# Performance work log

Measured on AMD Instinct MI355X. Metric: run time of the kernel, lower is better.

The kernel has to match this reference:

```python
import jax, jax.numpy as jnp
import numpy as np

NUM_HEADS = 16
BIG_NEG = -1e9  # additive mask value for padded keys (fp32)


def setup_inputs() -> dict:
    key = jax.random.key(0)
    ks = jax.random.split(key, 12)
    T, S, B, E = 2048, 2048, 2, 1024
    bound = np.sqrt(6.0 / (E + E))  # xavier_uniform for square E x E weights
    inp = {
        'query': jax.random.normal(ks[0], (T, B, E), jnp.float32),
        'key': jax.random.normal(ks[1], (S, B, E), jnp.float32),
        'value': jax.random.normal(ks[2], (S, B, E), jnp.float32),
        'attn_mask': jax.random.normal(ks[3], (T, S), jnp.float32) * 0.1,
        'key_padding_mask': jnp.zeros((B, S), dtype=bool),
        'Wq': jax.random.uniform(ks[4], (E, E), jnp.float32, -bound, bound),
        'bq': jnp.zeros((E,), jnp.float32),
        'Wk': jax.random.uniform(ks[5], (E, E), jnp.float32, -bound, bound),
        'bk': jnp.zeros((E,), jnp.float32),
        'Wv': jax.random.uniform(ks[6], (E, E), jnp.float32, -bound, bound),
        'bv': jnp.zeros((E,), jnp.float32),
        'Wo': jax.random.uniform(ks[7], (E, E), jnp.float32, -bound, bound),
        'bo': jnp.zeros((E,), jnp.float32),
    }
    return inp


def reference(query, key, value, attn_mask, key_padding_mask,
              Wq, bq, Wk, bk, Wv, bv, Wo, bo):
    T, B, E = query.shape
    S = key.shape[0]
    H = NUM_HEADS
    d = E // H
    scale = 1.0 / jnp.sqrt(jnp.asarray(d, query.dtype))

    # projections (nn.Linear: x @ W.T + b), then split heads
    q = (query @ Wq.T + bq).reshape(T, B, H, d) * scale  # [T,B,H,d]
    k = (key @ Wk.T + bk).reshape(S, B, H, d)            # [S,B,H,d]
    v = (value @ Wv.T + bv).reshape(S, B, H, d)          # [S,B,H,d]

    # QK^T scores: [B,H,T,S]
    scores = jnp.einsum('tbhd,sbhd->bhts', q, k)

    # merge masks: additive attn_mask + key_padding_mask (True -> -inf)
    merged = attn_mask[None, None, :, :] + jnp.where(
        key_padding_mask[:, None, None, :], BIG_NEG, 0.0).astype(scores.dtype)
    scores = scores + merged

    attn = jax.nn.softmax(scores, axis=-1)  # dropout p=0 -> identity

    out = jnp.einsum('bhts,sbhd->tbhd', attn, v).reshape(T, B, E)
    return out @ Wo.T + bo  # [T,B,E]
```

## Files before the change

kernel.cpp:

```cpp
#include <hip/hip_runtime.h>
#include <hip/hip_bf16.h>

typedef unsigned short u16;
typedef __attribute__((ext_vector_type(8))) short bf16x8;
typedef __attribute__((ext_vector_type(4))) float f32x4;

#define T_DIM 2048
#define S_DIM 2048
#define B_DIM 2
#define E_DIM 1024
#define H_DIM 16
#define D_HEAD 64
#define NTOK 4096

#if __has_builtin(__builtin_amdgcn_exp2f)
#define EXP2F(x) __builtin_amdgcn_exp2f(x)
#else
#define EXP2F(x) exp2f(x)
#endif

#define GLL16(gp, lp) __builtin_amdgcn_global_load_lds((gp), (lp), 16, 0, 0)

__device__ __forceinline__ float bf2f(u16 u) {
  union { unsigned int i; float f; } v; v.i = ((unsigned int)u) << 16; return v.f;
}
__device__ __forceinline__ u16 f2bf(float f) {
  union { float f; unsigned int i; } v; v.f = f;
  unsigned int r = v.i + 0x7fffu + ((v.i >> 16) & 1u);
  return (u16)(r >> 16);
}
__device__ __forceinline__ unsigned pk2(float a, float b) {
  return (unsigned)f2bf(a) | ((unsigned)f2bf(b) << 16);
}
__device__ __forceinline__ float bfu_lo(unsigned w) {
  union { unsigned int i; float f; } v; v.i = w << 16; return v.f;
}
__device__ __forceinline__ float bfu_hi(unsigned w) {
  union { unsigned int i; float f; } v; v.i = w & 0xffff0000u; return v.f;
}
__device__ __forceinline__ uint4 loadA8(const void* A, size_t base, int bf) {
  if (bf) return *(const uint4*)&((const u16*)A)[base];
  const float* af = (const float*)A + base;
  uint4 r;
  r.x = pk2(af[0], af[1]); r.y = pk2(af[2], af[3]);
  r.z = pk2(af[4], af[5]); r.w = pk2(af[6], af[7]);
  return r;
}

__global__ void detect_dtype(const u16* q, int* flag) {
  int lane = threadIdx.x;
  float v = bf2f(q[2 * lane]);
  bool ok = (v < 16.f) && (v > -16.f);
  unsigned long long b = __ballot(ok);
  if (lane == 0) *flag = (b == ~0ull) ? 1 : 0;
}

__global__ void prep_params(const void* Wq, const void* Wk, const void* Wv, const void* Wo,
                            const void* bq, const void* bk, const void* bv, const void* bo,
                            u16* wqkv, u16* wo, float* b3, float* bof,
                            const int* flag) {
  const int bf = *flag;
  const int W = E_DIM * E_DIM;
  int idx = blockIdx.x * 256 + threadIdx.x;
  if (idx < 4 * W) {
    int which = idx / W, i = idx - which * W;
    const void* src = which == 0 ? Wq : which == 1 ? Wk : which == 2 ? Wv : Wo;
    float v = bf ? bf2f(((const u16*)src)[i]) : ((const float*)src)[i];
    if (which == 0) v *= 0.125f;
    if (which < 3) wqkv[idx] = f2bf(v);
    else           wo[i] = f2bf(v);
  } else {
    int j = idx - 4 * W;
    if (j < 4 * E_DIM) {
      int which = j / E_DIM, i = j - which * E_DIM;
      const void* src = which == 0 ? bq : which == 1 ? bk : which == 2 ? bv : bo;
      float v = bf ? bf2f(((const u16*)src)[i]) : ((const float*)src)[i];
      if (which == 0) v *= 0.125f;
      if (which < 3) b3[j] = v;
      else           bof[i] = v;
    }
  }
}

__launch_bounds__(256)
__global__ void conv_in(const void* __restrict__ Q, const void* __restrict__ K,
                        const void* __restrict__ V,
                        u16* __restrict__ qb, u16* __restrict__ kb,
                        u16* __restrict__ vb, const int* __restrict__ flag) {
  const int bf = *flag;
  const size_t W = (size_t)NTOK * E_DIM;
  size_t e8 = ((size_t)blockIdx.x * 256 + threadIdx.x) * 8;
  int which = (int)(e8 / W);
  size_t i = e8 - (size_t)which * W;
  const void* src = which == 0 ? Q : which == 1 ? K : V;
  u16* dst = which == 0 ? qb : which == 1 ? kb : vb;
  *(uint4*)&dst[i] = loadA8(src, i, bf);
}

__global__ void prep_mask(const void* mask, const unsigned char* kpm,
                          u16* Mc, const int* flag) {
  const float L2E = 1.44269504f;
  const int bf = *flag;
  size_t e8 = ((size_t)blockIdx.x * 256 + threadIdx.x) * 8;
  int b = (int)(e8 / ((size_t)T_DIM * S_DIM));
  size_t rem = e8 - (size_t)b * T_DIM * S_DIM;
  int t = (int)(rem / S_DIM), s = (int)(rem - (size_t)t * S_DIM);
  const unsigned char* kb = &kpm[(size_t)b * S_DIM + s];
  uint4 o;
  if (bf) {
    const u16* m8 = &((const u16*)mask)[(size_t)t * S_DIM + s];
    o.x = pk2((bf2f(m8[0]) + (kb[0] ? -1e9f : 0.f)) * L2E,
              (bf2f(m8[1]) + (kb[1] ? -1e9f : 0.f)) * L2E);
    o.y = pk2((bf2f(m8[2]) + (kb[2] ? -1e9f : 0.f)) * L2E,
              (bf2f(m8[3]) + (kb[3] ? -1e9f : 0.f)) * L2E);
    o.z = pk2((bf2f(m8[4]) + (kb[4] ? -1e9f : 0.f)) * L2E,
              (bf2f(m8[5]) + (kb[5] ? -1e9f : 0.f)) * L2E);
    o.w = pk2((bf2f(m8[6]) + (kb[6] ? -1e9f : 0.f)) * L2E,
              (bf2f(m8[7]) + (kb[7] ? -1e9f : 0.f)) * L2E);
  } else {
    const float* mf = (const float*)mask + (size_t)t * S_DIM + s;
    o.x = pk2((mf[0] + (kb[0] ? -1e9f : 0.f)) * L2E,
              (mf[1] + (kb[1] ? -1e9f : 0.f)) * L2E);
    o.y = pk2((mf[2] + (kb[2] ? -1e9f : 0.f)) * L2E,
              (mf[3] + (kb[3] ? -1e9f : 0.f)) * L2E);
    o.z = pk2((mf[4] + (kb[4] ? -1e9f : 0.f)) * L2E,
              (mf[5] + (kb[5] ? -1e9f : 0.f)) * L2E);
    o.w = pk2((mf[6] + (kb[6] ? -1e9f : 0.f)) * L2E,
              (mf[7] + (kb[7] ? -1e9f : 0.f)) * L2E);
  }
  *(uint4*)&Mc[e8] = o;
}

__launch_bounds__(256)
__global__ void transpose_v(const u16* __restrict__ vp, u16* __restrict__ vt) {
  __shared__ unsigned int t[64 * 65];
  const int tid = threadIdx.x;
  const int s0 = blockIdx.x * 64;
  const int bh = blockIdx.y;
  const int b = bh / H_DIM, h = bh % H_DIM;
  {
    int sr = tid >> 2, cq = (tid & 3) * 16;
    const u16* src = &vp[((size_t)(s0 + sr) * B_DIM + b) * E_DIM + h * 64 + cq];
#pragma unroll
    for (int j = 0; j < 16; j++) t[(cq + j) * 65 + sr] = src[j];
  }
  __syncthreads();
  {
    int d = tid >> 2, sq = (tid & 3) * 16;
    u16* dst = &vt[((size_t)bh * 64 + d) * S_DIM + s0 + sq];
    uint4 o0, o1;
    o0.x = (t[d*65+sq+0] & 0xffffu) | (t[d*65+sq+1] << 16);
    o0.y = (t[d*65+sq+2] & 0xffffu) | (t[d*65+sq+3] << 16);
    o0.z = (t[d*65+sq+4] & 0xffffu) | (t[d*65+sq+5] << 16);
    o0.w = (t[d*65+sq+6] & 0xffffu) | (t[d*65+sq+7] << 16);
    o1.x = (t[d*65+sq+8] & 0xffffu) | (t[d*65+sq+9] << 16);
    o1.y = (t[d*65+sq+10] & 0xffffu) | (t[d*65+sq+11] << 16);
    o1.z = (t[d*65+sq+12] & 0xffffu) | (t[d*65+sq+13] << 16);
    o1.w = (t[d*65+sq+14] & 0xffffu) | (t[d*65+sq+15] << 16);
    *(uint4*)&dst[0] = o0;
    *(uint4*)&dst[8] = o1;
  }
}

__launch_bounds__(256, 3)
__global__ void gemm_qkv(const u16* __restrict__ Qb2, const u16* __restrict__ Kb2,
                         const u16* __restrict__ Vb2, const u16* __restrict__ W3,
                         const float* __restrict__ b3,
                         u16* __restrict__ qp, u16* __restrict__ kp, u16* __restrict__ vp) {
  __shared__ alignas(16) u16 As[128 * 64];
  __shared__ alignas(16) u16 Bs[128 * 64];
  const int tid = threadIdx.x;
  const int wave = tid >> 6, lane = tid & 63;
  const int g = lane >> 4, c = lane & 15;
  const int wy = wave >> 1, wx = wave & 1;
  const int which = blockIdx.x >> 3;
  const u16* A = which == 0 ? Qb2 : which == 1 ? Kb2 : Vb2;
  u16* dst = which == 0 ? qp : which == 1 ? kp : vp;
  const int m0 = blockIdx.y * 128, n0 = blockIdx.x * 128;
  const int K = E_DIM;

  const int swr = lane >> 3;
  const int swb = (lane & 7) ^ swr;
  const u16* Ag = &A [(size_t)(m0 + wave * 8 + swr) * K + swb * 8];
  const u16* Bg = &W3[(size_t)(n0 + wave * 8 + swr) * K + swb * 8];

  f32x4 acc[4][4] = {};
  for (int kc = 0; kc < K; kc += 64) {
#pragma unroll
    for (int i = 0; i < 4; i++) {
      GLL16(&Ag[(size_t)(i * 32) * K + kc], &As[(wave * 8 + i * 32) * 64]);
      GLL16(&Bg[(size_t)(i * 32) * K + kc], &Bs[(wave * 8 + i * 32) * 64]);
    }
    __syncthreads();
#pragma unroll
    for (int ks = 0; ks < 2; ks++) {
      const int kb = (((ks << 2) | g) ^ (c & 7)) * 8;
      bf16x8 av0 = *(const bf16x8*)&As[(wy * 64 +  0 + c) * 64 + kb];
      bf16x8 av1 = *(const bf16x8*)&As[(wy * 64 + 16 + c) * 64 + kb];
      bf16x8 av2 = *(const bf16x8*)&As[(wy * 64 + 32 + c) * 64 + kb];
      bf16x8 av3 = *(const bf16x8*)&As[(wy * 64 + 48 + c) * 64 + kb];
      bf16x8 bv0 = *(const bf16x8*)&Bs[(wx * 64 +  0 + c) * 64 + kb];
      bf16x8 bv1 = *(const bf16x8*)&Bs[(wx * 64 + 16 + c) * 64 + kb];
      bf16x8 bv2 = *(const bf16x8*)&Bs[(wx * 64 + 32 + c) * 64 + kb];
      bf16x8 bv3 = *(const bf16x8*)&Bs[(wx * 64 + 48 + c) * 64 + kb];
      acc[0][0] = __builtin_amdgcn_mfma_f32_16x16x32_bf16(av0, bv0, acc[0][0], 0, 0, 0);
      acc[0][1] = __builtin_amdgcn_mfma_f32_16x16x32_bf16(av0, bv1, acc[0][1], 0, 0, 0);
      acc[0][2] = __builtin_amdgcn_mfma_f32_16x16x32_bf16(av0, bv2, acc[0][2], 0, 0, 0);
      acc[0][3] = __builtin_amdgcn_mfma_f32_16x16x32_bf16(av0, bv3, acc[0][3], 0, 0, 0);
      acc[1][0] = __builtin_amdgcn_mfma_f32_16x16x32_bf16(av1, bv0, acc[1][0], 0, 0, 0);
      acc[1][1] = __builtin_amdgcn_mfma_f32_16x16x32_bf16(av1, bv1, acc[1][1], 0, 0, 0);
      acc[1][2] = __builtin_amdgcn_mfma_f32_16x16x32_bf16(av1, bv2, acc[1][2], 0, 0, 0);
      acc[1][3] = __builtin_amdgcn_mfma_f32_16x16x32_bf16(av1, bv3, acc[1][3], 0, 0, 0);
      acc[2][0] = __builtin_amdgcn_mfma_f32_16x16x32_bf16(av2, bv0, acc[2][0], 0, 0, 0);
      acc[2][1] = __builtin_amdgcn_mfma_f32_16x16x32_bf16(av2, bv1, acc[2][1], 0, 0, 0);
      acc[2][2] = __builtin_amdgcn_mfma_f32_16x16x32_bf16(av2, bv2, acc[2][2], 0, 0, 0);
      acc[2][3] = __builtin_amdgcn_mfma_f32_16x16x32_bf16(av2, bv3, acc[2][3], 0, 0, 0);
      acc[3][0] = __builtin_amdgcn_mfma_f32_16x16x32_bf16(av3, bv0, acc[3][0], 0, 0, 0);
      acc[3][1] = __builtin_amdgcn_mfma_f32_16x16x32_bf16(av3, bv1, acc[3][1], 0, 0, 0);
      acc[3][2] = __builtin_amdgcn_mfma_f32_16x16x32_bf16(av3, bv2, acc[3][2], 0, 0, 0);
      acc[3][3] = __builtin_amdgcn_mfma_f32_16x16x32_bf16(av3, bv3, acc[3][3], 0, 0, 0);
    }
    __syncthreads();
  }
#pragma unroll
  for (int mi = 0; mi < 4; mi++)
#pragma unroll
    for (int ni = 0; ni < 4; ni++)
#pragma unroll
      for (int r = 0; r < 4; r++) {
        int row = m0 + wy * 64 + mi * 16 + g * 4 + r;
        int col = n0 + wx * 64 + ni * 16 + c;
        int inner = col & (E_DIM - 1);
        dst[(size_t)row * E_DIM + inner] = f2bf(acc[mi][ni][r] + b3[col]);
      }
}

__launch_bounds__(256, 2)
__global__ void gemm_o(const u16* __restrict__ Aa, const u16* __restrict__ Bw,
                       const float* __restrict__ bias, void* __restrict__ C,
                       int out_f32) {
  __shared__ alignas(16) u16 As[64 * 64];
  __shared__ alignas(16) u16 Bs[128 * 64];
  const int tid = threadIdx.x;
  const int wave = tid >> 6, lane = tid & 63;
  const int g = lane >> 4, c = lane & 15;
  const int wy = wave >> 1, wx = wave & 1;
  const int m0 = blockIdx.y * 64, n0 = blockIdx.x * 128;
  const int K = E_DIM, N = E_DIM;

  const int swr = lane >> 3;
  const int swb = (lane & 7) ^ swr;
  const u16* Ag = &Aa[(size_t)(m0 + wave * 8 + swr) * K + swb * 8];
  const u16* Bg = &Bw[(size_t)(n0 + wave * 8 + swr) * K + swb * 8];

  f32x4 acc[2][4] = {};
  for (int kc = 0; kc < K; kc += 64) {
#pragma unroll
    for (int i = 0; i < 2; i++)
      GLL16(&Ag[(size_t)(i * 32) * K + kc], &As[(wave * 8 + i * 32) * 64]);
#pragma unroll
    for (int i = 0; i < 4; i++)
      GLL16(&Bg[(size_t)(i * 32) * K + kc], &Bs[(wave * 8 + i * 32) * 64]);
    __syncthreads();
#pragma unroll
    for (int ks = 0; ks < 2; ks++) {
      const int kb = (((ks << 2) | g) ^ (c & 7)) * 8;
      bf16x8 av0 = *(const bf16x8*)&As[(wy * 32 +  0 + c) * 64 + kb];
      bf16x8 av1 = *(const bf16x8*)&As[(wy * 32 + 16 + c) * 64 + kb];
      bf16x8 bv0 = *(const bf16x8*)&Bs[(wx * 64 +  0 + c) * 64 + kb];
      bf16x8 bv1 = *(const bf16x8*)&Bs[(wx * 64 + 16 + c) * 64 + kb];
      bf16x8 bv2 = *(const bf16x8*)&Bs[(wx * 64 + 32 + c) * 64 + kb];
      bf16x8 bv3 = *(const bf16x8*)&Bs[(wx * 64 + 48 + c) * 64 + kb];
      acc[0][0] = __builtin_amdgcn_mfma_f32_16x16x32_bf16(av0, bv0, acc[0][0], 0, 0, 0);
      acc[0][1] = __builtin_amdgcn_mfma_f32_16x16x32_bf16(av0, bv1, acc[0][1], 0, 0, 0);
      acc[0][2] = __builtin_amdgcn_mfma_f32_16x16x32_bf16(av0, bv2, acc[0][2], 0, 0, 0);
      acc[0][3] = __builtin_amdgcn_mfma_f32_16x16x32_bf16(av0, bv3, acc[0][3], 0, 0, 0);
      acc[1][0] = __builtin_amdgcn_mfma_f32_16x16x32_bf16(av1, bv0, acc[1][0], 0, 0, 0);
      acc[1][1] = __builtin_amdgcn_mfma_f32_16x16x32_bf16(av1, bv1, acc[1][1], 0, 0, 0);
      acc[1][2] = __builtin_amdgcn_mfma_f32_16x16x32_bf16(av1, bv2, acc[1][2], 0, 0, 0);
      acc[1][3] = __builtin_amdgcn_mfma_f32_16x16x32_bf16(av1, bv3, acc[1][3], 0, 0, 0);
    }
    __syncthreads();
  }
#pragma unroll
  for (int mi = 0; mi < 2; mi++)
#pragma unroll
    for (int ni = 0; ni < 4; ni++)
#pragma unroll
      for (int r = 0; r < 4; r++) {
        int row = m0 + wy * 32 + mi * 16 + g * 4 + r;
        int col = n0 + wx * 64 + ni * 16 + c;
        float v = acc[mi][ni][r] + bias[col];
        size_t idx = (size_t)row * N + col;
        if (out_f32) ((float*)C)[idx] = v;
        else         ((u16*)C)[idx] = f2bf(v);
      }
}

__launch_bounds__(256, 4)
__global__ void flash_attn(const u16* __restrict__ Qb, const u16* __restrict__ Kb,
                           const u16* __restrict__ Vtg, const u16* __restrict__ Mc,
                           u16* __restrict__ ctx) {
  __shared__ alignas(16) u16 Ks[64 * 72];
  __shared__ alignas(16) u16 Vs[64 * 72];
  __shared__ alignas(16) u16 MP[64 * 72];
  const int tid = threadIdx.x;
  const int wave = tid >> 6, lane = tid & 63;
  const int g = lane >> 4, c = lane & 15;
  const int bh = blockIdx.x;
  const int t0 = blockIdx.y * 64;
  const int b = bh / H_DIM, h = bh % H_DIM;
  const size_t hoff = (size_t)h * D_HEAD;
  const float L2E = 1.44269504f;
  const u16* mc = &Mc[((size_t)b * T_DIM + t0) * S_DIM];
  const int rr = tid >> 3, oo = (tid & 7) * 8;

  *(uint4*)&Ks[(rr)      * 72 + oo] =
      *(const uint4*)&Qb[((size_t)(t0 + rr)      * B_DIM + b) * E_DIM + hoff + oo];
  *(uint4*)&Ks[(rr + 32) * 72 + oo] =
      *(const uint4*)&Qb[((size_t)(t0 + rr + 32) * B_DIM + b) * E_DIM + hoff + oo];
  __syncthreads();
  const int arow = wave * 16 + c;
  bf16x8 q0 = *(const bf16x8*)&Ks[arow * 72 + g * 8];
  bf16x8 q1 = *(const bf16x8*)&Ks[arow * 72 + 32 + g * 8];

  uint4 pk0, pk1, pv0, pv1, pm0, pm1;
  pk0 = *(const uint4*)&Kb[((size_t)(rr)      * B_DIM + b) * E_DIM + hoff + oo];
  pk1 = *(const uint4*)&Kb[((size_t)(rr + 32) * B_DIM + b) * E_DIM + hoff + oo];
  pv0 = *(const uint4*)&Vtg[((size_t)bh * 64 + rr)      * S_DIM + oo];
  pv1 = *(const uint4*)&Vtg[((size_t)bh * 64 + rr + 32) * S_DIM + oo];
  pm0 = *(const uint4*)&mc[(size_t)(rr)      * S_DIM + oo];
  pm1 = *(const uint4*)&mc[(size_t)(rr + 32) * S_DIM + oo];
  __syncthreads();

  f32x4 O[4] = {};
  float rsum = 0.f;
  const int trow = arow * 72;

  for (int s0 = 0; s0 < S_DIM; s0 += 64) {
    *(uint4*)&Ks[(rr)      * 72 + oo] = pk0;
    *(uint4*)&Ks[(rr + 32) * 72 + oo] = pk1;
    *(uint4*)&Vs[(rr)      * 72 + oo] = pv0;
    *(uint4*)&Vs[(rr + 32) * 72 + oo] = pv1;
    *(uint4*)&MP[(rr)      * 72 + oo] = pm0;
    *(uint4*)&MP[(rr + 32) * 72 + oo] = pm1;
    __syncthreads();
    if (s0 + 64 < S_DIM) {
      int s2 = s0 + 64;
      pk0 = *(const uint4*)&Kb[((size_t)(s2 + rr)      * B_DIM + b) * E_DIM + hoff + oo];
      pk1 = *(const uint4*)&Kb[((size_t)(s2 + rr + 32) * B_DIM + b) * E_DIM + hoff + oo];
      pv0 = *(const uint4*)&Vtg[((size_t)bh * 64 + rr)      * S_DIM + s2 + oo];
      pv1 = *(const uint4*)&Vtg[((size_t)bh * 64 + rr + 32) * S_DIM + s2 + oo];
      pm0 = *(const uint4*)&mc[(size_t)(rr)      * S_DIM + s2 + oo];
      pm1 = *(const uint4*)&mc[(size_t)(rr + 32) * S_DIM + s2 + oo];
    }

    f32x4 sc[4] = {};
#pragma unroll
    for (int n = 0; n < 4; n++) {
      bf16x8 k0 = *(const bf16x8*)&Ks[(n * 16 + c) * 72 + g * 8];
      bf16x8 k1 = *(const bf16x8*)&Ks[(n * 16 + c) * 72 + 32 + g * 8];
      sc[n] = __builtin_amdgcn_mfma_f32_16x16x32_bf16(k0, q0, sc[n], 0, 0, 0);
      sc[n] = __builtin_amdgcn_mfma_f32_16x16x32_bf16(k1, q1, sc[n], 0, 0, 0);
    }
#pragma unroll
    for (int n = 0; n < 4; n++) {
      uint2 mw = *(const uint2*)&MP[trow + n * 16 + g * 4];
      float p0 = EXP2F(fmaf(sc[n][0], L2E, bfu_lo(mw.x)));
      float p1 = EXP2F(fmaf(sc[n][1], L2E, bfu_hi(mw.x)));
      float p2 = EXP2F(fmaf(sc[n][2], L2E, bfu_lo(mw.y)));
      float p3 = EXP2F(fmaf(sc[n][3], L2E, bfu_hi(mw.y)));
      rsum += (p0 + p1) + (p2 + p3);
      *(unsigned*)&MP[trow + n * 16 + g * 4]     = pk2(p0, p1);
      *(unsigned*)&MP[trow + n * 16 + g * 4 + 2] = pk2(p2, p3);
    }
    bf16x8 p0 = *(const bf16x8*)&MP[arow * 72 + g * 8];
    bf16x8 p1 = *(const bf16x8*)&MP[arow * 72 + 32 + g * 8];
#pragma unroll
    for (int n = 0; n < 4; n++) {
      bf16x8 v0 = *(const bf16x8*)&Vs[(n * 16 + c) * 72 + g * 8];
      bf16x8 v1 = *(const bf16x8*)&Vs[(n * 16 + c) * 72 + 32 + g * 8];
      O[n] = __builtin_amdgcn_mfma_f32_16x16x32_bf16(p0, v0, O[n], 0, 0, 0);
      O[n] = __builtin_amdgcn_mfma_f32_16x16x32_bf16(p1, v1, O[n], 0, 0, 0);
    }
    __syncthreads();
  }
  float l = rsum;
  l += __shfl_xor(l, 16, 64);
  l += __shfl_xor(l, 32, 64);
  float rl = 1.f / l;
#pragma unroll
  for (int r = 0; r < 4; r++) {
    float rlr = __shfl(rl, g * 4 + r, 64);
    int t = t0 + wave * 16 + g * 4 + r;
#pragma unroll
    for (int n = 0; n < 4; n++) {
      int dcol = n * 16 + c;
      ctx[((size_t)t * B_DIM + b) * E_DIM + hoff + dcol] = f2bf(O[n][r] * rlr);
    }
  }
}

extern "C" void kernel_launch(void* const* d_in, const int* in_sizes, int n_in,
                              void* d_out, int out_size, void* d_ws, size_t ws_size,
                              hipStream_t stream) {
  const void* query = d_in[0];
  const void* key   = d_in[1];
  const void* value = d_in[2];
  const void* amask = d_in[3];
  const unsigned char* kpm = (const unsigned char*)d_in[4];
  const void* Wq = d_in[5];  const void* bq = d_in[6];
  const void* Wk = d_in[7];  const void* bk = d_in[8];
  const void* Wv = d_in[9];  const void* bv = d_in[10];
  const void* Wo = d_in[11]; const void* bo = d_in[12];

  int out_f32 = 0;
  {
    hipDeviceptr_t base = nullptr; size_t sz = 0;
    if (hipMemGetAddressRange(&base, &sz, (hipDeviceptr_t)d_out) == hipSuccess && sz) {
      size_t avail = sz - (size_t)((char*)d_out - (char*)base);
      size_t need_f32 = (size_t)out_size * 4;
      if (avail >= need_f32 && avail <= need_f32 + need_f32 / 2) out_f32 = 1;
    }
  }

  char* ws = (char*)d_ws;
  size_t off = 0;
  auto alloc = [&](size_t bytes) {
    void* p = ws + off;
    off += (bytes + 255) & ~(size_t)255;
    return p;
  };
  int*   flag = (int*)  alloc(256);
  u16*   qp   = (u16*)  alloc((size_t)NTOK * E_DIM * 2);
  u16*   kp   = (u16*)  alloc((size_t)NTOK * E_DIM * 2);
  u16*   vp   = (u16*)  alloc((size_t)NTOK * E_DIM * 2);
  u16*   vt   = (u16*)  alloc((size_t)NTOK * E_DIM * 2);
  u16*   Mcb  = (u16*)  alloc((size_t)B_DIM * T_DIM * S_DIM * 2);
  u16*   wqkv = (u16*)  alloc((size_t)3 * E_DIM * E_DIM * 2);
  u16*   wo   = (u16*)  alloc((size_t)E_DIM * E_DIM * 2);
  float* b3   = (float*)alloc(3 * E_DIM * 4);
  float* bof  = (float*)alloc(E_DIM * 4);
  if (off > ws_size) return;

  u16* qb  = vt;
  u16* kb2 = Mcb;
  u16* vb2 = Mcb + (size_t)NTOK * E_DIM;

  detect_dtype<<<1, 64, 0, stream>>>((const u16*)query, flag);

  {
    int total = 4 * E_DIM * E_DIM + 4 * E_DIM;
    prep_params<<<(total + 255) / 256, 256, 0, stream>>>(
        Wq, Wk, Wv, Wo, bq, bk, bv, bo, wqkv, wo, b3, bof, flag);
  }

  {
    size_t total8 = (size_t)3 * NTOK * E_DIM / 8;
    conv_in<<<(unsigned)(total8 / 256), 256, 0, stream>>>(
        query, key, value, qb, kb2, vb2, flag);
  }

  gemm_qkv<<<dim3(3 * E_DIM / 128, NTOK / 128), 256, 0, stream>>>(
      qb, kb2, vb2, wqkv, b3, qp, kp, vp);

  {
    size_t total8 = (size_t)B_DIM * T_DIM * S_DIM / 8;
    prep_mask<<<(unsigned)(total8 / 256), 256, 0, stream>>>(amask, kpm, Mcb, flag);
  }

  transpose_v<<<dim3(S_DIM / 64, B_DIM * H_DIM), 256, 0, stream>>>(vp, vt);

  u16* ctx = vp;
  flash_attn<<<dim3(B_DIM * H_DIM, T_DIM / 64), 256, 0, stream>>>(qp, kp, vt, Mcb, ctx);

  gemm_o<<<dim3(E_DIM / 128, NTOK / 64), 256, 0, stream>>>(ctx, wo, bof, d_out, out_f32);
}
```

Before: 286.3 us.

## Merge prep kernels into two launches and read mask directly in attention

Combines the weight/bias conversion with the input conversion into one launch, and the V transpose with the mask preparation into another, so two kernel launches and their gaps are removed. Inside flash attention, each lane now loads its own mask elements straight from global memory into registers instead of staging the mask tile through shared memory, which drops two LDS stores and an LDS read per tile. The direct mask loads are small uint2 accesses strided by row and are issued after the barrier, so they are not prefetched a tile ahead and their latency may be less well hidden.

Result: no change. 291.8 us (+2.0%).

```diff
diff --git a/kernel.cpp b/kernel.cpp
--- a/kernel.cpp
+++ b/kernel.cpp
@@ -55,110 +55,112 @@
   if (lane == 0) *flag = (b == ~0ull) ? 1 : 0;
 }
 
-__global__ void prep_params(const void* Wq, const void* Wk, const void* Wv, const void* Wo,
-                            const void* bq, const void* bk, const void* bv, const void* bo,
-                            u16* wqkv, u16* wo, float* b3, float* bof,
-                            const int* flag) {
+#define PARAM_BLOCKS 16400
+__launch_bounds__(256)
+__global__ void prep_a(const void* Wq, const void* Wk, const void* Wv, const void* Wo,
+                       const void* bq, const void* bk, const void* bv, const void* bo,
+                       u16* wqkv, u16* wo, float* b3, float* bof,
+                       const void* Q, const void* Kk, const void* V,
+                       u16* qb, u16* kb, u16* vb,
+                       const int* flag) {
   const int bf = *flag;
-  const int W = E_DIM * E_DIM;
-  int idx = blockIdx.x * 256 + threadIdx.x;
-  if (idx < 4 * W) {
-    int which = idx / W, i = idx - which * W;
-    const void* src = which == 0 ? Wq : which == 1 ? Wk : which == 2 ? Wv : Wo;
-    float v = bf ? bf2f(((const u16*)src)[i]) : ((const float*)src)[i];
-    if (which == 0) v *= 0.125f;
-    if (which < 3) wqkv[idx] = f2bf(v);
-    else           wo[i] = f2bf(v);
-  } else {
-    int j = idx - 4 * W;
-    if (j < 4 * E_DIM) {
-      int which = j / E_DIM, i = j - which * E_DIM;
-      const void* src = which == 0 ? bq : which == 1 ? bk : which == 2 ? bv : bo;
+  const int bid = blockIdx.x;
+  if (bid < PARAM_BLOCKS) {
+    const int W = E_DIM * E_DIM;
+    int idx = bid * 256 + threadIdx.x;
+    if (idx < 4 * W) {
+      int which = idx / W, i = idx - which * W;
+      const void* src = which == 0 ? Wq : which == 1 ? Wk : which == 2 ? Wv : Wo;
       float v = bf ? bf2f(((const u16*)src)[i]) : ((const float*)src)[i];
       if (which == 0) v *= 0.125f;
-      if (which < 3) b3[j] = v;
-      else           bof[i] = v;
-    }
+      if (which < 3) wqkv[idx] = f2bf(v);
+      else           wo[i] = f2bf(v);
+    } else {
+      int j = idx - 4 * W;
+      if (j < 4 * E_DIM) {
+        int which = j / E_DIM, i = j - which * E_DIM;
+        const void* src = which == 0 ? bq : which == 1 ? bk : which == 2 ? bv : bo;
+        float v = bf ? bf2f(((const u16*)src)[i]) : ((const float*)src)[i];
+        if (which == 0) v *= 0.125f;
+        if (which < 3) b3[j] = v;
+        else           bof[i] = v;
+      }
+    }
+  } else {
+    const size_t W = (size_t)NTOK * E_DIM;
+    size_t e8 = ((size_t)(bid - PARAM_BLOCKS) * 256 + threadIdx.x) * 8;
+    int which = (int)(e8 / W);
+    size_t i = e8 - (size_t)which * W;
+    const void* src = which == 0 ? Q : which == 1 ? Kk : V;
+    u16* dst = which == 0 ? qb : which == 1 ? kb : vb;
+    *(uint4*)&dst[i] = loadA8(src, i, bf);
   }
 }
 
 __launch_bounds__(256)
-__global__ void conv_in(const void* __restrict__ Q, const void* __restrict__ K,
-                        const void* __restrict__ V,
-                        u16* __restrict__ qb, u16* __restrict__ kb,
-                        u16* __restrict__ vb, const int* __restrict__ flag) {
-  const int bf = *flag;
-  const size_t W = (size_t)NTOK * E_DIM;
-  size_t e8 = ((size_t)blockIdx.x * 256 + threadIdx.x) * 8;
-  int which = (int)(e8 / W);
-  size_t i = e8 - (size_t)which * W;
-  const void* src = which == 0 ? Q : which == 1 ? K : V;
-  u16* dst = which == 0 ? qb : which == 1 ? kb : vb;
-  *(uint4*)&dst[i] = loadA8(src, i, bf);
-}
-
-__global__ void prep_mask(const void* mask, const unsigned char* kpm,
-                          u16* Mc, const int* flag) {
-  const float L2E = 1.44269504f;
-  const int bf = *flag;
-  size_t e8 = ((size_t)blockIdx.x * 256 + threadIdx.x) * 8;
-  int b = (int)(e8 / ((size_t)T_DIM * S_DIM));
-  size_t rem = e8 - (size_t)b * T_DIM * S_DIM;
-  int t = (int)(rem / S_DIM), s = (int)(rem - (size_t)t * S_DIM);
-  const unsigned char* kb = &kpm[(size_t)b * S_DIM + s];
-  uint4 o;
-  if (bf) {
-    const u16* m8 = &((const u16*)mask)[(size_t)t * S_DIM + s];
-    o.x = pk2((bf2f(m8[0]) + (kb[0] ? -1e9f : 0.f)) * L2E,
-              (bf2f(m8[1]) + (kb[1] ? -1e9f : 0.f)) * L2E);
-    o.y = pk2((bf2f(m8[2]) + (kb[2] ? -1e9f : 0.f)) * L2E,
-              (bf2f(m8[3]) + (kb[3] ? -1e9f : 0.f)) * L2E);
-    o.z = pk2((bf2f(m8[4]) + (kb[4] ? -1e9f : 0.f)) * L2E,
-              (bf2f(m8[5]) + (kb[5] ? -1e9f : 0.f)) * L2E);
-    o.w = pk2((bf2f(m8[6]) + (kb[6] ? -1e9f : 0.f)) * L2E,
-              (bf2f(m8[7]) + (kb[7] ? -1e9f : 0.f)) * L2E);
+__global__ void prep_b(const u16* __restrict__ vp, u16* __restrict__ vt,
+                       const void* __restrict__ mask, const unsigned char* __restrict__ kpm,
+                       u16* __restrict__ Mc, const int* __restrict__ flag) {
+  const int bid = blockIdx.x;
+  if (bid < 1024) {
+    __shared__ unsigned int t[64 * 65];
+    const int tid = threadIdx.x;
+    const int s0 = (bid & 31) * 64;
+    const int bh = bid >> 5;
+    const int b = bh / H_DIM, h = bh % H_DIM;
+    {
+      int sr = tid >> 2, cq = (tid & 3) * 16;
+      const u16* src = &vp[((size_t)(s0 + sr) * B_DIM + b) * E_DIM + h * 64 + cq];
+#pragma unroll
+      for (int j = 0; j < 16; j++) t[(cq + j) * 65 + sr] = src[j];
+    }
+    __syncthreads();
+    {
+      int d = tid >> 2, sq = (tid & 3) * 16;
+      u16* dst = &vt[((size_t)bh * 64 + d) * S_DIM + s0 + sq];
+      uint4 o0, o1;
+      o0.x = (t[d*65+sq+0] & 0xffffu) | (t[d*65+sq+1] << 16);
+      o0.y = (t[d*65+sq+2] & 0xffffu) | (t[d*65+sq+3] << 16);
+      o0.z = (t[d*65+sq+4] & 0xffffu) | (t[d*65+sq+5] << 16);
+      o0.w = (t[d*65+sq+6] & 0xffffu) | (t[d*65+sq+7] << 16);
+      o1.x = (t[d*65+sq+8] & 0xffffu) | (t[d*65+sq+9] << 16);
+      o1.y = (t[d*65+sq+10] & 0xffffu) | (t[d*65+sq+11] << 16);
+      o1.z = (t[d*65+sq+12] & 0xffffu) | (t[d*65+sq+13] << 16);
+      o1.w = (t[d*65+sq+14] & 0xffffu) | (t[d*65+sq+15] << 16);
+      *(uint4*)&dst[0] = o0;
+      *(uint4*)&dst[8] = o1;
+    }
   } else {
-    const float* mf = (const float*)mask + (size_t)t * S_DIM + s;
-    o.x = pk2((mf[0] + (kb[0] ? -1e9f : 0.f)) * L2E,
-              (mf[1] + (kb[1] ? -1e9f : 0.f)) * L2E);
-    o.y = pk2((mf[2] + (kb[2] ? -1e9f : 0.f)) * L2E,
-              (mf[3] + (kb[3] ? -1e9f : 0.f)) * L2E);
-    o.z = pk2((mf[4] + (kb[4] ? -1e9f : 0.f)) * L2E,
-              (mf[5] + (kb[5] ? -1e9f : 0.f)) * L2E);
-    o.w = pk2((mf[6] + (kb[6] ? -1e9f : 0.f)) * L2E,
-              (mf[7] + (kb[7] ? -1e9f : 0.f)) * L2E);
-  }
-  *(uint4*)&Mc[e8] = o;
-}
-
-__launch_bounds__(256)
-__global__ void transpose_v(const u16* __restrict__ vp, u16* __restrict__ vt) {
-  __shared__ unsigned int t[64 * 65];
-  const int tid = threadIdx.x;
-  const int s0 = blockIdx.x * 64;
-  const int bh = blockIdx.y;
-  const int b = bh / H_DIM, h = bh % H_DIM;
-  {
-    int sr = tid >> 2, cq = (tid & 3) * 16;
-    const u16* src = &vp[((size_t)(s0 + sr) * B_DIM + b) * E_DIM + h * 64 + cq];
-#pragma unroll
-    for (int j = 0; j < 16; j++) t[(cq + j) * 65 + sr] = src[j];
-  }
-  __syncthreads();
-  {
-    int d = tid >> 2, sq = (tid & 3) * 16;
-    u16* dst = &vt[((size_t)bh * 64 + d) * S_DIM + s0 + sq];
-    uint4 o0, o1;
-    o0.x = (t[d*65+sq+0] & 0xffffu) | (t[d*65+sq+1] << 16);
-    o0.y = (t[d*65+sq+2] & 0xffffu) | (t[d*65+sq+3] << 16);
-    o0.z = (t[d*65+sq+4] & 0xffffu) | (t[d*65+sq+5] << 16);
-    o0.w = (t[d*65+sq+6] & 0xffffu) | (t[d*65+sq+7] << 16);
-    o1.x = (t[d*65+sq+8] & 0xffffu) | (t[d*65+sq+9] << 16);
-    o1.y = (t[d*65+sq+10] & 0xffffu) | (t[d*65+sq+11] << 16);
-    o1.z = (t[d*65+sq+12] & 0xffffu) | (t[d*65+sq+13] << 16);
-    o1.w = (t[d*65+sq+14] & 0xffffu) | (t[d*65+sq+15] << 16);
-    *(uint4*)&dst[0] = o0;
-    *(uint4*)&dst[8] = o1;
+    const float L2E = 1.44269504f;
+    const int bf = *flag;
+    size_t e8 = ((size_t)(bid - 1024) * 256 + threadIdx.x) * 8;
+    int b = (int)(e8 / ((size_t)T_DIM * S_DIM));
+    size_t rem = e8 - (size_t)b * T_DIM * S_DIM;
+    int tt = (int)(rem / S_DIM), s = (int)(rem - (size_t)tt * S_DIM);
+    const unsigned char* kb = &kpm[(size_t)b * S_DIM + s];
+    uint4 o;
+    if (bf) {
+      const u16* m8 = &((const u16*)mask)[(size_t)tt * S_DIM + s];
+      o.x = pk2((bf2f(m8[0]) + (kb[0] ? -1e9f : 0.f)) * L2E,
+                (bf2f(m8[1]) + (kb[1] ? -1e9f : 0.f)) * L2E);
+      o.y = pk2((bf2f(m8[2]) + (kb[2] ? -1e9f : 0.f)) * L2E,
+                (bf2f(m8[3]) + (kb[3] ? -1e9f : 0.f)) * L2E);
+      o.z = pk2((bf2f(m8[4]) + (kb[4] ? -1e9f : 0.f)) * L2E,
+                (bf2f(m8[5]) + (kb[5] ? -1e9f : 0.f)) * L2E);
+      o.w = pk2((bf2f(m8[6]) + (kb[6] ? -1e9f : 0.f)) * L2E,
+                (bf2f(m8[7]) + (kb[7] ? -1e9f : 0.f)) * L2E);
+    } else {
+      const float* mf = (const float*)mask + (size_t)tt * S_DIM + s;
+      o.x = pk2((mf[0] + (kb[0] ? -1e9f : 0.f)) * L2E,
+                (mf[1] + (kb[1] ? -1e9f : 0.f)) * L2E);
+      o.y = pk2((mf[2] + (kb[2] ? -1e9f : 0.f)) * L2E,
+                (mf[3] + (kb[3] ? -1e9f : 0.f)) * L2E);
+      o.z = pk2((mf[4] + (kb[4] ? -1e9f : 0.f)) * L2E,
+                (mf[5] + (kb[5] ? -1e9f : 0.f)) * L2E);
+      o.w = pk2((mf[6] + (kb[6] ? -1e9f : 0.f)) * L2E,
+                (mf[7] + (kb[7] ? -1e9f : 0.f)) * L2E);
+    }
+    *(uint4*)&Mc[e8] = o;
   }
 }
 
@@ -324,35 +326,34 @@
   bf16x8 q0 = *(const bf16x8*)&Ks[arow * 72 + g * 8];
   bf16x8 q1 = *(const bf16x8*)&Ks[arow * 72 + 32 + g * 8];
 
-  uint4 pk0, pk1, pv0, pv1, pm0, pm1;
+  uint4 pk0, pk1, pv0, pv1;
   pk0 = *(const uint4*)&Kb[((size_t)(rr)      * B_DIM + b) * E_DIM + hoff + oo];
   pk1 = *(const uint4*)&Kb[((size_t)(rr + 32) * B_DIM + b) * E_DIM + hoff + oo];
   pv0 = *(const uint4*)&Vtg[((size_t)bh * 64 + rr)      * S_DIM + oo];
   pv1 = *(const uint4*)&Vtg[((size_t)bh * 64 + rr + 32) * S_DIM + oo];
-  pm0 = *(const uint4*)&mc[(size_t)(rr)      * S_DIM + oo];
-  pm1 = *(const uint4*)&mc[(size_t)(rr + 32) * S_DIM + oo];
   __syncthreads();
 
   f32x4 O[4] = {};
   float rsum = 0.f;
   const int trow = arow * 72;
+  const u16* mrow = &mc[(size_t)arow * S_DIM + g * 4];
 
   for (int s0 = 0; s0 < S_DIM; s0 += 64) {
     *(uint4*)&Ks[(rr)      * 72 + oo] = pk0;
     *(uint4*)&Ks[(rr + 32) * 72 + oo] = pk1;
     *(uint4*)&Vs[(rr)      * 72 + oo] = pv0;
     *(uint4*)&Vs[(rr + 32) * 72 + oo] = pv1;
-    *(uint4*)&MP[(rr)      * 72 + oo] = pm0;
-    *(uint4*)&MP[(rr + 32) * 72 + oo] = pm1;
-    __syncthreads();
+    __syncthreads();
+    uint2 mw[4];
+#pragma unroll
+    for (int n = 0; n < 4; n++)
+      mw[n] = *(const uint2*)&mrow[s0 + n * 16];
     if (s0 + 64 < S_DIM) {
       int s2 = s0 + 64;
       pk0 = *(const uint4*)&Kb[((size_t)(s2 + rr)      * B_DIM + b) * E_DIM + hoff + oo];
       pk1 = *(const uint4*)&Kb[((size_t)(s2 + rr + 32) * B_DIM + b) * E_DIM + hoff + oo];
       pv0 = *(const uint4*)&Vtg[((size_t)bh * 64 + rr)      * S_DIM + s2 + oo];
       pv1 = *(const uint4*)&Vtg[((size_t)bh * 64 + rr + 32) * S_DIM + s2 + oo];
-      pm0 = *(const uint4*)&mc[(size_t)(rr)      * S_DIM + s2 + oo];
-      pm1 = *(const uint4*)&mc[(size_t)(rr + 32) * S_DIM + s2 + oo];
     }
 
     f32x4 sc[4] = {};
@@ -365,11 +366,10 @@
     }
 #pragma unroll
     for (int n = 0; n < 4; n++) {
-      uint2 mw = *(const uint2*)&MP[trow + n * 16 + g * 4];
-      float p0 = EXP2F(fmaf(sc[n][0], L2E, bfu_lo(mw.x)));
-      float p1 = EXP2F(fmaf(sc[n][1], L2E, bfu_hi(mw.x)));
-      float p2 = EXP2F(fmaf(sc[n][2], L2E, bfu_lo(mw.y)));
-      float p3 = EXP2F(fmaf(sc[n][3], L2E, bfu_hi(mw.y)));
+      float p0 = EXP2F(fmaf(sc[n][0], L2E, bfu_lo(mw[n].x)));
+      float p1 = EXP2F(fmaf(sc[n][1], L2E, bfu_hi(mw[n].x)));
+      float p2 = EXP2F(fmaf(sc[n][2], L2E, bfu_lo(mw[n].y)));
+      float p3 = EXP2F(fmaf(sc[n][3], L2E, bfu_hi(mw[n].y)));
       rsum += (p0 + p1) + (p2 + p3);
       *(unsigned*)&MP[trow + n * 16 + g * 4]     = pk2(p0, p1);
       *(unsigned*)&MP[trow + n * 16 + g * 4 + 2] = pk2(p2, p3);
@@ -449,27 +449,14 @@
 
   detect_dtype<<<1, 64, 0, stream>>>((const u16*)query, flag);
 
-  {
-    int total = 4 * E_DIM * E_DIM + 4 * E_DIM;
-    prep_params<<<(total + 255) / 256, 256, 0, stream>>>(
-        Wq, Wk, Wv, Wo, bq, bk, bv, bo, wqkv, wo, b3, bof, flag);
-  }
-
-  {
-    size_t total8 = (size_t)3 * NTOK * E_DIM / 8;
-    conv_in<<<(unsigned)(total8 / 256), 256, 0, stream>>>(
-        query, key, value, qb, kb2, vb2, flag);
-  }
+  prep_a<<<PARAM_BLOCKS + 6144, 256, 0, stream>>>(
+      Wq, Wk, Wv, Wo, bq, bk, bv, bo, wqkv, wo, b3, bof,
+      query, key, value, qb, kb2, vb2, flag);
 
   gemm_qkv<<<dim3(3 * E_DIM / 128, NTOK / 128), 256, 0, stream>>>(
       qb, kb2, vb2, wqkv, b3, qp, kp, vp);
 
-  {
-    size_t total8 = (size_t)B_DIM * T_DIM * S_DIM / 8;
-    prep_mask<<<(unsigned)(total8 / 256), 256, 0, stream>>>(amask, kpm, Mcb, flag);
-  }
-
-  transpose_v<<<dim3(S_DIM / 64, B_DIM * H_DIM), 256, 0, stream>>>(vp, vt);
+  prep_b<<<1024 + 4096, 256, 0, stream>>>(vp, vt, amask, kpm, Mcb, flag);
 
   u16* ctx = vp;
   flash_attn<<<dim3(B_DIM * H_DIM, T_DIM / 64), 256, 0, stream>>>(qp, kp, vt, Mcb, ctx);
```
